# Optimization experiments

Hardware: AMD Instinct MI355X
Metric: run time of the kernel (lower is better)

Reference implementation:

```python
import math
import jax, jax.numpy as jnp
import numpy as np

# ---- static config (matches init_kwargs) ----
B, L, D = 32, 1024, 256
H = 4
E = D // H          # head dim = 64
LF = L // 2 + 1     # rfft bins = 513
LEFT, RIGHT = 205, 513   # retained freq band: int(LF*(1-0.6)) .. LF  (i=0, global mixer)
SPATIAL_RATIO = 0.1
TOP_K = int(5 * math.log(L))  # factor=5 -> 34
LN_EPS = 1e-8


def _layer_norm(x, g, b):
    m = jnp.mean(x, axis=-1, keepdims=True)
    v = jnp.mean((x - m) ** 2, axis=-1, keepdims=True)
    return (x - m) / jnp.sqrt(v + LN_EPS) * g + b


def _gelu_erf(x):
    return x * 0.5 * (1.0 + jax.lax.erf(x / math.sqrt(2.0)))


def _time_delay_agg_training(values, corr):
    # values, corr: [B,H,E,L]; shared top-k delay indices across batch (training path)
    mean_value = jnp.mean(corr, axis=(1, 2))                  # [B,L]
    _, index = jax.lax.top_k(jnp.mean(mean_value, axis=0), TOP_K)  # [TOP_K] int32
    weights = mean_value[:, index]                            # [B,TOP_K]
    tmp_corr = jax.nn.softmax(weights, axis=-1)               # [B,TOP_K]
    t = jnp.arange(L)

    def body(acc, args):
        idx, w = args                                         # idx: scalar delay, w: [B]
        pattern = jnp.take(values, (t + idx) % L, axis=-1)    # roll(values, -idx, axis=-1)
        return acc + pattern * w[:, None, None, None], None

    acc, _ = jax.lax.scan(body, jnp.zeros_like(values), (index, tmp_corr.T))
    return acc                                                # [B,H,E,L]


def setup_inputs() -> dict:
    key = jax.random.key(0)
    ks = jax.random.split(key, 12)
    lin = lambda k: jax.random.normal(k, (D, D), jnp.float32) * 0.02  # stored [in,out]
    return {
        "x": jax.random.normal(ks[0], (B, L, D), jnp.float32),
        "Wq": lin(ks[1]), "bq": jnp.zeros((D,), jnp.float32),
        "Wk": lin(ks[2]), "bk": jnp.zeros((D,), jnp.float32),
        "Wv": lin(ks[3]), "bv": jnp.zeros((D,), jnp.float32),
        "Wd": lin(ks[4]), "bd": jnp.zeros((D,), jnp.float32),
        "ln1_g": jnp.ones((D,), jnp.float32), "ln1_b": jnp.zeros((D,), jnp.float32),
        "W1": lin(ks[5]), "b1": jnp.zeros((D,), jnp.float32),
        "W2": lin(ks[6]), "b2": jnp.zeros((D,), jnp.float32),
        "ln2_g": jnp.ones((D,), jnp.float32), "ln2_b": jnp.zeros((D,), jnp.float32),
    }


def reference(x, Wq, bq, Wk, bk, Wv, bv, Wd, bd, ln1_g, ln1_b, W1, b1, W2, b2, ln2_g, ln2_b):
    # ---- HybridAttention ----
    q = (x @ Wq + bq).reshape(B, L, H, E).transpose(0, 2, 3, 1)  # [B,H,E,L]
    k = (x @ Wk + bk).reshape(B, L, H, E).transpose(0, 2, 3, 1)
    v = (x @ Wv + bv).reshape(B, L, H, E).transpose(0, 2, 3, 1)

    q_fft = jnp.fft.rfft(q, axis=-1)      # [B,H,E,LF]
    k_fft = jnp.fft.rfft(k, axis=-1)
    mask = jnp.zeros((LF,), jnp.float32).at[LEFT:RIGHT].set(1.0)

    # band-limited autocorrelation (equivalent to the index-box scatter/gather)
    corr = jnp.fft.irfft(q_fft * jnp.conj(k_fft) * mask, n=L, axis=-1)  # [B,H,E,L]
    Vt = _time_delay_agg_training(v, corr)                              # [B,H,E,L]
    context_time = Vt.transpose(0, 3, 1, 2).reshape(B, L, D)

    # spatial (band-pass filtered) attention branch
    v_fft = jnp.fft.rfft(v, axis=-1)
    qs = jnp.fft.irfft(q_fft * mask, n=L, axis=-1).transpose(0, 1, 3, 2)  # [B,H,L,E]
    ks_ = jnp.fft.irfft(k_fft * mask, n=L, axis=-1).transpose(0, 1, 3, 2)
    vs = jnp.fft.irfft(v_fft * mask, n=L, axis=-1).transpose(0, 1, 3, 2)
    scores = jnp.einsum('bhle,bhse->bhls', qs, ks_) / math.sqrt(E)
    probs = jax.nn.softmax(scores, axis=-1)
    ctx_sp = jnp.einsum('bhls,bhse->bhle', probs, vs).transpose(0, 2, 1, 3).reshape(B, L, D)

    context = (1.0 - SPATIAL_RATIO) * context_time + SPATIAL_RATIO * ctx_sp
    h = _layer_norm(context @ Wd + bd + x, ln1_g, ln1_b)

    # ---- FeedForward ----
    f = _gelu_erf(h @ W1 + b1) @ W2 + b2
    return _layer_norm(f + h, ln2_g, ln2_b)
```

## Files before the change

kernel.cpp:

```cpp
#include <hip/hip_runtime.h>
#include <hip/hip_bf16.h>
#include <math.h>

#define Lc 1024
#define Dc 256
#define Bc 32
#define Hc 4
#define Ec 64
#define TOPK 34
#define LEFTc 205

typedef unsigned short u16;
typedef __attribute__((ext_vector_type(8))) short bf16x8;
typedef __attribute__((ext_vector_type(4))) float f32x4;

__device__ __forceinline__ float bf2f(u16 u) {
    return __uint_as_float(((unsigned)u) << 16);
}
__device__ __forceinline__ u16 f2bf(float f) {
    unsigned u = __float_as_uint(f);
    u += 0x7FFFu + ((u >> 16) & 1u);
    return (u16)(u >> 16);
}

__global__ void detect_k(const u16* __restrict__ x, int* __restrict__ flag) {
    __shared__ int cnt;
    if (threadIdx.x == 0) cnt = 0;
    __syncthreads();
    int bad = 0;
    for (int i = threadIdx.x; i < 4096; i += 256) {
        float a = fabsf(bf2f(x[i]));
        if (!(a == 0.0f || (a >= 1e-8f && a <= 1e8f))) bad++;
    }
    atomicAdd(&cnt, bad);
    __syncthreads();
    if (threadIdx.x == 0) *flag = (cnt > 512) ? 1 : 0;
}

struct SrcPtrs { const void* p[17]; };
__global__ __launch_bounds__(256) void ingest_all_k(
    SrcPtrs sp, u16* __restrict__ cx, u16* __restrict__ wts, const int* __restrict__ flag)
{
    const long NB = (long)Bc * Lc * Dc;
    long i = (long)blockIdx.x * 256 + threadIdx.x;
    const int fp = *flag;
    const void* src; u16* dst; long off;
    if (i < NB) {
        src = sp.p[0]; dst = cx; off = i;
    } else {
        long j = i - NB;
        if (j < 6L * 65536) {
            const int w = (int)(j >> 16); off = j & 65535;
            const int wsidx[6] = {1, 3, 5, 7, 11, 13};
            src = sp.p[wsidx[w]]; dst = wts + (long)w * 65536;
        } else {
            long k2 = j - 6L * 65536;
            if (k2 >= 2560) return;
            const int v = (int)(k2 >> 8); off = k2 & 255;
            const int vsidx[10] = {2, 4, 6, 8, 9, 10, 12, 14, 15, 16};
            src = sp.p[vsidx[v]]; dst = wts + 6L * 65536 + (long)v * 256;
        }
    }
    dst[off] = fp ? f2bf(((const float*)src)[off]) : ((const u16*)src)[off];
}

__global__ void build_h(float* __restrict__ hf) {
    int d = blockIdx.x * blockDim.x + threadIdx.x;
    if (d >= Lc) return;
    float s = 0.f;
    for (int f = LEFTc; f < 512; ++f) {
        int m = (f * d) & (Lc - 1);
        s += __cosf((float)m * 6.135923151542565e-3f);
    }
    float ny = (d & 1) ? -1.f : 1.f;
    hf[d] = (2.f * s + ny) * (1.f / 1024.f);
}

__global__ void build_G(const float* __restrict__ hf, u16* __restrict__ G) {
    int i = blockIdx.x * 256 + threadIdx.x;
    int t = i >> 10, s = i & (Lc - 1);
    G[i] = f2bf(hf[(t - s) & (Lc - 1)]);
}

__global__ __launch_bounds__(256) void transpose_k(
    const u16* __restrict__ in, u16* __restrict__ out)
{
    __shared__ u16 t[32][33];
    const int l0 = blockIdx.x * 32, d0 = blockIdx.y * 32, b = blockIdx.z;
    const int tx = threadIdx.x & 31, ty = threadIdx.x >> 5;
    const u16* ib = in + (size_t)b * Lc * Dc;
    #pragma unroll
    for (int i = 0; i < 4; ++i)
        t[ty + i * 8][tx] = ib[(size_t)(l0 + ty + i * 8) * Dc + d0 + tx];
    __syncthreads();
    u16* ob = out + (size_t)b * Dc * Lc;
    #pragma unroll
    for (int i = 0; i < 4; ++i)
        ob[(size_t)(d0 + ty + i * 8) * Lc + l0 + tx] = t[tx][ty + i * 8];
}

__global__ __launch_bounds__(256) void wtrans_k(
    const u16* __restrict__ src, u16* __restrict__ dst)
{
    __shared__ u16 t[32][33];
    const int c0 = blockIdx.x * 32, r0 = blockIdx.y * 32;
    const u16* s = src + (size_t)blockIdx.z * 65536;
    u16* d = dst + (size_t)blockIdx.z * 65536;
    const int tx = threadIdx.x & 31, ty = threadIdx.x >> 5;
    #pragma unroll
    for (int i = 0; i < 4; ++i)
        t[ty + i * 8][tx] = s[(r0 + ty + i * 8) * 256 + c0 + tx];
    __syncthreads();
    #pragma unroll
    for (int i = 0; i < 4; ++i)
        d[(c0 + ty + i * 8) * 256 + r0 + tx] = t[tx][ty + i * 8];
}

template <int EPI, bool ACOMB>
__global__ __launch_bounds__(256) void mgemm_k(
    const u16* __restrict__ Abase, const u16* __restrict__ A2base,
    const u16* __restrict__ BTbase, const u16* __restrict__ bias,
    const u16* __restrict__ resid, u16* __restrict__ Cbase,
    int M, int N, int K, long strA, long strBT, long strC)
{
    const int z = blockIdx.z;
    const u16* A  = Abase + (size_t)z * strA;
    const u16* BT = BTbase + (size_t)z * strBT;
    u16* C        = Cbase + (size_t)z * strC;
    const int tid = threadIdx.x;
    const int wave = tid >> 6, lane = tid & 63;
    const int m16 = lane & 15, quad = lane >> 4;
    const int m0 = blockIdx.y * 128 + wave * 32;
    const int n0 = blockIdx.x * 64;

    __shared__ __align__(16) u16 sB[8192];

    const u16* arow0 = A + (size_t)(m0 + m16) * K + quad * 8;
    const u16* arow1 = arow0 + (size_t)16 * K;
    const u16* a2row0 = ACOMB ? (A2base + (size_t)z * strA + (size_t)(m0 + m16) * K + quad * 8) : nullptr;
    const u16* a2row1 = ACOMB ? (a2row0 + (size_t)16 * K) : nullptr;

    const u16* bgp[4];
    u16* bls[4];
    #pragma unroll
    for (int i = 0; i < 4; ++i) {
        const int c = tid + i * 256;
        const int nr = c >> 4, ko = c & 15;
        bgp[i] = BT + (size_t)(n0 + nr) * K + ko * 8;
        bls[i] = sB + ((nr >> 4) * 4 + (ko >> 2)) * 512 + (ko & 3) * 128
                    + (((nr & 15) ^ (ko & 3))) * 8;
    }

    bf16x8 breg[4];
    #pragma unroll
    for (int i = 0; i < 4; ++i) breg[i] = *(const bf16x8*)(bgp[i]);

    f32x4 acc[2][4] = {};

    #pragma unroll 1
    for (int kc = 0; kc < K; kc += 128) {
        #pragma unroll
        for (int i = 0; i < 4; ++i) *(bf16x8*)(bls[i]) = breg[i];
        __syncthreads();
        if (kc + 128 < K) {
            #pragma unroll
            for (int i = 0; i < 4; ++i) breg[i] = *(const bf16x8*)(bgp[i] + kc + 128);
        }
        #pragma unroll
        for (int kf = 0; kf < 4; ++kf) {
            bf16x8 a0 = *(const bf16x8*)(arow0 + kc + kf * 32);
            bf16x8 a1 = *(const bf16x8*)(arow1 + kc + kf * 32);
            if (ACOMB) {
                const bf16x8 x0 = *(const bf16x8*)(a2row0 + kc + kf * 32);
                const bf16x8 x1 = *(const bf16x8*)(a2row1 + kc + kf * 32);
                #pragma unroll
                for (int j = 0; j < 8; ++j) {
                    a0[j] = (short)f2bf(0.9f * bf2f((u16)a0[j]) + 0.1f * bf2f((u16)x0[j]));
                    a1[j] = (short)f2bf(0.9f * bf2f((u16)a1[j]) + 0.1f * bf2f((u16)x1[j]));
                }
            }
            #pragma unroll
            for (int nt = 0; nt < 4; ++nt) {
                const bf16x8 bf = *(const bf16x8*)(sB + (nt * 4 + kf) * 512 + quad * 128
                                                      + ((m16 ^ quad)) * 8);
                acc[0][nt] = __builtin_amdgcn_mfma_f32_16x16x32_bf16(a0, bf, acc[0][nt], 0, 0, 0);
                acc[1][nt] = __builtin_amdgcn_mfma_f32_16x16x32_bf16(a1, bf, acc[1][nt], 0, 0, 0);
            }
        }
        __syncthreads();
    }

    #pragma unroll
    for (int ms = 0; ms < 2; ++ms) {
        #pragma unroll
        for (int nt = 0; nt < 4; ++nt) {
            const int col = n0 + nt * 16 + m16;
            const float bv = bias ? bf2f(bias[col]) : 0.f;
            #pragma unroll
            for (int r = 0; r < 4; ++r) {
                const size_t off = (size_t)(m0 + ms * 16 + quad * 4 + r) * N + col;
                float v = acc[ms][nt][r] + bv;
                if (EPI == 1) v += bf2f(resid[off]);
                if (EPI == 2) v = 0.5f * v * (1.0f + erff(v * 0.70710678118654752f));
                C[off] = f2bf(v);
            }
        }
    }
}

__global__ __launch_bounds__(256) void corr_k(
    const u16* __restrict__ qs, const u16* __restrict__ ks, float* __restrict__ mv)
{
    const int l = blockIdx.x;
    const int b = ((l & 7) << 2) | ((l >> 3) & 3);
    const int rest = l >> 5;
    const int g = rest & 15;
    const int uq = rest >> 4;
    const int wave = threadIdx.x >> 6, lane = threadIdx.x & 63;
    const int m16 = lane & 15, quad = lane >> 4;
    const size_t base = (size_t)b * Lc * Dc;

    __shared__ float red[4][124];
    for (int i = threadIdx.x; i < 4 * 124; i += 256) ((float*)red)[i] = 0.f;
    __syncthreads();

    f32x4 acc[4] = {};
    #pragma unroll
    for (int ui = 0; ui < 4; ++ui) {
        const int u = uq * 16 + wave * 4 + ui;
        const u16* qrow = qs + base + (size_t)(u * 16 + m16) * Dc + quad * 8;
        const u16* kr[4];
        #pragma unroll
        for (int al = 0; al < 4; ++al) {
            const int s = (u - g * 4 - al) & 63;
            kr[al] = ks + base + (size_t)(s * 16 + m16) * Dc + quad * 8;
        }
        #pragma unroll
        for (int k0 = 0; k0 < Dc; k0 += 32) {
            const bf16x8 aq = *(const bf16x8*)(qrow + k0);
            #pragma unroll
            for (int al = 0; al < 4; ++al) {
                const bf16x8 bk = *(const bf16x8*)(kr[al] + k0);
                acc[al] = __builtin_amdgcn_mfma_f32_16x16x32_bf16(aq, bk, acc[al], 0, 0, 0);
            }
        }
    }

    #pragma unroll
    for (int al = 0; al < 4; ++al)
        #pragma unroll
        for (int r = 0; r < 4; ++r)
            atomicAdd(&red[wave][al * 31 + quad * 4 + r - m16 + 15], acc[al][r]);
    __syncthreads();

    if (threadIdx.x < 124) {
        const int al = threadIdx.x / 31, dd = threadIdx.x % 31;
        const float s = red[0][threadIdx.x] + red[1][threadIdx.x] +
                        red[2][threadIdx.x] + red[3][threadIdx.x];
        atomicAdd(&mv[b * Lc + (((g * 4 + al) * 16 + dd - 15) & (Lc - 1))], s);
    }
}

__global__ __launch_bounds__(256) void attn_k(
    const u16* __restrict__ qs, const u16* __restrict__ ks,
    const u16* __restrict__ vsT, u16* __restrict__ ctx)
{
    const int lt = blockIdx.x, h = blockIdx.y, b = blockIdx.z;

    __shared__ __align__(16) u16 sK[8192];
    __shared__ __align__(16) u16 sV[8192];
    __shared__ __align__(16) u16 sP[8192];

    const int tid  = threadIdx.x;
    const int wave = tid >> 6;
    const int lane = tid & 63;
    const int m16  = lane & 15;
    const int quad = lane >> 4;
    const int l0   = lt * 64;
    const size_t base = (size_t)b * Lc * Dc + (size_t)h * Ec;
    const size_t vtbase = ((size_t)b * Dc + (size_t)h * Ec) * Lc;

    const u16* qrow = qs + base + (size_t)(l0 + wave * 16 + m16) * Dc + quad * 8;
    const bf16x8 qa0 = *(const bf16x8*)(qrow);
    const bf16x8 qa1 = *(const bf16x8*)(qrow + 32);

    const u16* kgp[4]; const u16* vgp[4];
    u16* kls[4]; u16* vls[4];
    #pragma unroll
    for (int i = 0; i < 4; ++i) {
        const int c = tid + i * 256;
        const int sr = c >> 3, eo = c & 7;
        kgp[i] = ks + base + (size_t)sr * Dc + eo * 8;
        kls[i] = sK + ((sr >> 4) * 2 + (eo >> 2)) * 512 + (eo & 3) * 128
                    + (((sr & 15) ^ (eo & 3))) * 8;
        const int er = c >> 4, so = c & 15;
        vgp[i] = vsT + vtbase + (size_t)er * Lc + so * 8;
        vls[i] = sV + ((er >> 4) * 4 + (so >> 2)) * 512 + (so & 3) * 128
                    + (((er & 15) ^ (so & 3))) * 8;
    }

    bf16x8 kreg[4], vreg[4];
    #pragma unroll
    for (int i = 0; i < 4; ++i) {
        kreg[i] = *(const bf16x8*)(kgp[i]);
        vreg[i] = *(const bf16x8*)(vgp[i]);
    }

    f32x4 o[4] = {};
    float rs[4] = {0.f, 0.f, 0.f, 0.f};

    const int rsw = m16 ^ quad;
    const int hrd = ((quad & 1) << 1) | (m16 >> 3);
    const int prd = (m16 ^ hrd) * 8;

    #pragma unroll 1
    for (int s0 = 0; s0 < Lc; s0 += 128) {
        #pragma unroll
        for (int i = 0; i < 4; ++i) {
            *(bf16x8*)(kls[i]) = kreg[i];
            *(bf16x8*)(vls[i]) = vreg[i];
        }
        __syncthreads();
        if (s0 + 128 < Lc) {
            #pragma unroll
            for (int i = 0; i < 4; ++i) {
                kreg[i] = *(const bf16x8*)(kgp[i] + (size_t)(s0 + 128) * Dc);
                vreg[i] = *(const bf16x8*)(vgp[i] + (s0 + 128));
            }
        }

        #pragma unroll
        for (int st = 0; st < 8; ++st) {
            const bf16x8 kb0 = *(const bf16x8*)(sK + (st * 2 + 0) * 512 + quad * 128 + rsw * 8);
            const bf16x8 kb1 = *(const bf16x8*)(sK + (st * 2 + 1) * 512 + quad * 128 + rsw * 8);
            f32x4 c4 = {0.f, 0.f, 0.f, 0.f};
            c4 = __builtin_amdgcn_mfma_f32_16x16x32_bf16(qa0, kb0, c4, 0, 0, 0);
            c4 = __builtin_amdgcn_mfma_f32_16x16x32_bf16(qa1, kb1, c4, 0, 0, 0);
            const int q2 = ((st & 1) << 1) | (m16 >> 3);
            const int hst = ((q2 & 1) << 1) | (quad >> 1);
            u16* pw = sP + wave * 2048 + (st >> 1) * 512 + q2 * 128 + (m16 & 7);
            #pragma unroll
            for (int r = 0; r < 4; ++r) {
                const float p = __expf(c4[r] * 0.125f);
                rs[r] += p;
                pw[(((quad * 4 + r) ^ hst)) * 8] = f2bf(p);
            }
        }
        __syncthreads();

        const bf16x8 a0 = *(const bf16x8*)(sP + wave * 2048 + 0 * 512 + quad * 128 + prd);
        const bf16x8 a1 = *(const bf16x8*)(sP + wave * 2048 + 1 * 512 + quad * 128 + prd);
        const bf16x8 a2 = *(const bf16x8*)(sP + wave * 2048 + 2 * 512 + quad * 128 + prd);
        const bf16x8 a3 = *(const bf16x8*)(sP + wave * 2048 + 3 * 512 + quad * 128 + prd);
        #pragma unroll
        for (int nt = 0; nt < 4; ++nt) {
            o[nt] = __builtin_amdgcn_mfma_f32_16x16x32_bf16(a0, *(const bf16x8*)(sV + (nt * 4 + 0) * 512 + quad * 128 + rsw * 8), o[nt], 0, 0, 0);
            o[nt] = __builtin_amdgcn_mfma_f32_16x16x32_bf16(a1, *(const bf16x8*)(sV + (nt * 4 + 1) * 512 + quad * 128 + rsw * 8), o[nt], 0, 0, 0);
            o[nt] = __builtin_amdgcn_mfma_f32_16x16x32_bf16(a2, *(const bf16x8*)(sV + (nt * 4 + 2) * 512 + quad * 128 + rsw * 8), o[nt], 0, 0, 0);
            o[nt] = __builtin_amdgcn_mfma_f32_16x16x32_bf16(a3, *(const bf16x8*)(sV + (nt * 4 + 3) * 512 + quad * 128 + rsw * 8), o[nt], 0, 0, 0);
        }
        __syncthreads();
    }

    #pragma unroll
    for (int off = 1; off < 16; off <<= 1) {
        #pragma unroll
        for (int r = 0; r < 4; ++r) rs[r] += __shfl_xor(rs[r], off);
    }
    #pragma unroll
    for (int nt = 0; nt < 4; ++nt) {
        #pragma unroll
        for (int r = 0; r < 4; ++r)
            ctx[base + (size_t)(l0 + wave * 16 + quad * 4 + r) * Dc + nt * 16 + m16] =
                f2bf(o[nt][r] / rs[r]);
    }
}

__global__ __launch_bounds__(1024) void topk_k(
    const float* __restrict__ mv, int* __restrict__ idx_g, float* __restrict__ w_g)
{
    __shared__ float wvs[16];
    __shared__ int   wis[16];
    __shared__ int   widx;
    __shared__ int   sidx[TOPK];
    const int tid = threadIdx.x;
    const int lane = tid & 63;
    const int wv_id = tid >> 6;

    float g = 0.f;
    for (int b = 0; b < Bc; ++b) g += mv[b * Lc + tid];

    for (int j = 0; j < TOPK; ++j) {
        float v = g; int ix = tid;
        #pragma unroll
        for (int off = 32; off > 0; off >>= 1) {
            const float ov = __shfl_xor(v, off);
            const int   oi = __shfl_xor(ix, off);
            if (ov > v || (ov == v && oi < ix)) { v = ov; ix = oi; }
        }
        if (lane == 0) { wvs[wv_id] = v; wis[wv_id] = ix; }
        __syncthreads();
        if (tid == 0) {
            float bv = wvs[0]; int bi = wis[0];
            for (int u = 1; u < 16; ++u)
                if (wvs[u] > bv || (wvs[u] == bv && wis[u] < bi)) { bv = wvs[u]; bi = wis[u]; }
            widx = bi; sidx[j] = bi; idx_g[j] = bi;
        }
        __syncthreads();
        if (tid == widx) g = -3e38f;
        __syncthreads();
    }
    if (tid < Bc) {
        float wv[TOPK];
        float mx = -3e38f;
        for (int j = 0; j < TOPK; ++j) {
            wv[j] = mv[tid * Lc + sidx[j]] * (1.0f / (float)Dc);
            mx = fmaxf(mx, wv[j]);
        }
        float sum = 0.f;
        for (int j = 0; j < TOPK; ++j) { wv[j] = expf(wv[j] - mx); sum += wv[j]; }
        for (int j = 0; j < TOPK; ++j) w_g[tid * TOPK + j] = wv[j] / sum;
    }
}

__global__ __launch_bounds__(256) void agg_k(
    const u16* __restrict__ v, const int* __restrict__ idx,
    const float* __restrict__ w, u16* __restrict__ ct)
{
    const int b = blockIdx.y;
    const int t = blockIdx.x * 4 + (threadIdx.x >> 6);
    const int lane = threadIdx.x & 63;
    __shared__ int   sidx[TOPK];
    __shared__ float sw[TOPK];
    if (threadIdx.x < TOPK) { sidx[threadIdx.x] = idx[threadIdx.x]; sw[threadIdx.x] = w[b * TOPK + threadIdx.x]; }
    __syncthreads();
    const u16* vb = v + (size_t)b * Lc * Dc;
    const int c4 = lane * 4;
    float a0 = 0.f, a1 = 0.f, a2 = 0.f, a3 = 0.f;
    for (int j = 0; j < TOPK; ++j) {
        const float wj = sw[j];
        const ushort4 u = *reinterpret_cast<const ushort4*>(
            vb + (size_t)((t + sidx[j]) & (Lc - 1)) * Dc + c4);
        a0 += wj * bf2f(u.x); a1 += wj * bf2f(u.y);
        a2 += wj * bf2f(u.z); a3 += wj * bf2f(u.w);
    }
    ushort4 o; o.x = f2bf(a0); o.y = f2bf(a1); o.z = f2bf(a2); o.w = f2bf(a3);
    *reinterpret_cast<ushort4*>(ct + (size_t)b * Lc * Dc + (size_t)t * Dc + c4) = o;
}

template <bool FINAL>
__global__ __launch_bounds__(256) void ln_k(
    const u16* __restrict__ in, const u16* __restrict__ g,
    const u16* __restrict__ be, void* __restrict__ out, const int* __restrict__ flag)
{
    const int wave = threadIdx.x >> 6, lane = threadIdx.x & 63;
    const int row = blockIdx.x * 4 + wave;
    const int c4 = lane * 4;
    const ushort4 u = *reinterpret_cast<const ushort4*>(in + (size_t)row * Dc + c4);
    float x[4] = {bf2f(u.x), bf2f(u.y), bf2f(u.z), bf2f(u.w)};
    float sm = x[0] + x[1] + x[2] + x[3];
    float sq = x[0]*x[0] + x[1]*x[1] + x[2]*x[2] + x[3]*x[3];
    #pragma unroll
    for (int off = 1; off < 64; off <<= 1) {
        sm += __shfl_xor(sm, off);
        sq += __shfl_xor(sq, off);
    }
    const float mean = sm * (1.f / 256.f);
    const float var = sq * (1.f / 256.f) - mean * mean;
    const float rstd = __frsqrt_rn(var + 1e-8f);
    const ushort4 gg = *reinterpret_cast<const ushort4*>(g + c4);
    const ushort4 bb = *reinterpret_cast<const ushort4*>(be + c4);
    float y[4];
    y[0] = (x[0] - mean) * rstd * bf2f(gg.x) + bf2f(bb.x);
    y[1] = (x[1] - mean) * rstd * bf2f(gg.y) + bf2f(bb.y);
    y[2] = (x[2] - mean) * rstd * bf2f(gg.z) + bf2f(bb.z);
    y[3] = (x[3] - mean) * rstd * bf2f(gg.w) + bf2f(bb.w);
    if (FINAL && *flag) {
        float4 o = make_float4(y[0], y[1], y[2], y[3]);
        *reinterpret_cast<float4*>((float*)out + (size_t)row * Dc + c4) = o;
    } else {
        ushort4 o; o.x = f2bf(y[0]); o.y = f2bf(y[1]); o.z = f2bf(y[2]); o.w = f2bf(y[3]);
        *reinterpret_cast<ushort4*>((u16*)out + (size_t)row * Dc + c4) = o;
    }
}

extern "C" void kernel_launch(void* const* d_in, const int* in_sizes, int n_in,
                              void* d_out, int out_size, void* d_ws, size_t ws_size,
                              hipStream_t stream)
{
    (void)in_sizes; (void)n_in; (void)out_size; (void)ws_size;

    const size_t BLD = (size_t)Bc * Lc * Dc;
    const size_t SLOT = BLD * 2;
    const long LD = (long)(Lc * Dc);
    char* ws = (char*)d_ws;
    u16* b0 = (u16*)(ws + 0 * SLOT);
    u16* b1 = (u16*)(ws + 1 * SLOT);
    u16* b2 = (u16*)(ws + 2 * SLOT);
    u16* b3 = (u16*)(ws + 3 * SLOT);
    u16* cx = (u16*)(ws + 4 * SLOT);
    u16* G  = (u16*)(ws + 5 * SLOT);
    char* tail = ws + 5 * SLOT + (size_t)Lc * Lc * 2;
    u16* wts  = (u16*)tail;
    u16* wtsT = wts + 6 * 65536 + 10 * 256;
    char* tail2 = (char*)(wtsT + 6 * 65536);
    float* hf  = (float*)(tail2 + 512);
    float* mv  = hf + Lc;
    int*   idx = (int*)(mv + Bc * Lc);
    float* wsm = (float*)(idx + 64);
    int*   flag = (int*)(wsm + Bc * TOPK);

    u16* vecs = wts + 6 * 65536;
    u16* cbv = vecs + 2 * 256;  u16* cbd = vecs + 3 * 256;
    u16* l1g = vecs + 4 * 256;  u16* l1b = vecs + 5 * 256;
    u16* cb1 = vecs + 6 * 256;  u16* cb2 = vecs + 7 * 256;
    u16* l2g = vecs + 8 * 256;  u16* l2b = vecs + 9 * 256;
    u16* wvT = wtsT + 2 * 65536;
    u16* wdT = wtsT + 3 * 65536; u16* w1T = wtsT + 4 * 65536; u16* w2T = wtsT + 5 * 65536;

    detect_k<<<dim3(1), 256, 0, stream>>>((const u16*)d_in[0], flag);
    SrcPtrs sp;
    for (int i = 0; i < 17; ++i) sp.p[i] = d_in[i];
    ingest_all_k<<<dim3(34314), 256, 0, stream>>>(sp, cx, wts, flag);
    wtrans_k<<<dim3(8, 8, 6), 256, 0, stream>>>(wts, wtsT);

    build_h<<<dim3(4), 256, 0, stream>>>(hf);
    build_G<<<dim3((Lc * Lc) / 256), 256, 0, stream>>>(hf, G);

    transpose_k<<<dim3(32, 8, 32), 256, 0, stream>>>(cx, b1);
    mgemm_k<0, false><<<dim3(4, 8, 32), 256, 0, stream>>>(
        G, nullptr, b1, nullptr, nullptr, b0, Lc, Dc, Lc, 0, LD, LD);

    mgemm_k<0, false><<<dim3(4, 256, 3), 256, 0, stream>>>(
        b0, nullptr, wtsT, nullptr, nullptr, b1, Bc * Lc, Dc, Dc, 0, 65536, (long)BLD);

    hipMemsetAsync(mv, 0, (size_t)Bc * Lc * 4, stream);
    corr_k<<<dim3(2048), 256, 0, stream>>>(b1, b2, mv);

    transpose_k<<<dim3(32, 8, 32), 256, 0, stream>>>(b3, b0);
    attn_k<<<dim3(16, 4, 32), 256, 0, stream>>>(b1, b2, b0, b3);

    topk_k<<<dim3(1), 1024, 0, stream>>>(mv, idx, wsm);

    const dim3 gProj(4, 256, 1);
    mgemm_k<0, false><<<gProj, 256, 0, stream>>>(cx, nullptr, wvT, cbv, nullptr, b1, Bc * Lc, Dc, Dc, 0, 0, 0);
    agg_k<<<dim3(256, 32), 256, 0, stream>>>(b1, idx, wsm, b2);

    mgemm_k<1, true><<<gProj, 256, 0, stream>>>(b2, b3, wdT, cbd, cx, b0, Bc * Lc, Dc, Dc, 0, 0, 0);

    ln_k<false><<<dim3(8192), 256, 0, stream>>>(b0, l1g, l1b, b1, flag);

    mgemm_k<2, false><<<gProj, 256, 0, stream>>>(b1, nullptr, w1T, cb1, nullptr, b2, Bc * Lc, Dc, Dc, 0, 0, 0);
    mgemm_k<1, false><<<gProj, 256, 0, stream>>>(b2, nullptr, w2T, cb2, b1, b3, Bc * Lc, Dc, Dc, 0, 0, 0);

    ln_k<true><<<dim3(8192), 256, 0, stream>>>(b3, l2g, l2b, d_out, flag);
}
```

Measured before the change: 621.1 us.

## Fuse autocorrelation diagonal sums into attention score computation

Removes the separate corr_k kernel, which recomputed Q·K products to build per-lag correlation sums. The attention kernel now accumulates each raw score into a shared-memory per-lag array by wrapped diagonal and adds that array to the global mean-value buffer at the end. This reuses the score MFMAs already done for attention. In exchange it adds a shared atomic per score element plus a 4 KB shared array, and it sums per head rather than across all heads, so correctness depends on corr_k having computed the same per-head diagonal sums.

```diff
diff --git a/kernel.cpp b/kernel.cpp
--- a/kernel.cpp
+++ b/kernel.cpp
@@ -208,68 +208,16 @@
     }
 }
 
-__global__ __launch_bounds__(256) void corr_k(
-    const u16* __restrict__ qs, const u16* __restrict__ ks, float* __restrict__ mv)
-{
-    const int l = blockIdx.x;
-    const int b = ((l & 7) << 2) | ((l >> 3) & 3);
-    const int rest = l >> 5;
-    const int g = rest & 15;
-    const int uq = rest >> 4;
-    const int wave = threadIdx.x >> 6, lane = threadIdx.x & 63;
-    const int m16 = lane & 15, quad = lane >> 4;
-    const size_t base = (size_t)b * Lc * Dc;
-
-    __shared__ float red[4][124];
-    for (int i = threadIdx.x; i < 4 * 124; i += 256) ((float*)red)[i] = 0.f;
-    __syncthreads();
-
-    f32x4 acc[4] = {};
-    #pragma unroll
-    for (int ui = 0; ui < 4; ++ui) {
-        const int u = uq * 16 + wave * 4 + ui;
-        const u16* qrow = qs + base + (size_t)(u * 16 + m16) * Dc + quad * 8;
-        const u16* kr[4];
-        #pragma unroll
-        for (int al = 0; al < 4; ++al) {
-            const int s = (u - g * 4 - al) & 63;
-            kr[al] = ks + base + (size_t)(s * 16 + m16) * Dc + quad * 8;
-        }
-        #pragma unroll
-        for (int k0 = 0; k0 < Dc; k0 += 32) {
-            const bf16x8 aq = *(const bf16x8*)(qrow + k0);
-            #pragma unroll
-            for (int al = 0; al < 4; ++al) {
-                const bf16x8 bk = *(const bf16x8*)(kr[al] + k0);
-                acc[al] = __builtin_amdgcn_mfma_f32_16x16x32_bf16(aq, bk, acc[al], 0, 0, 0);
-            }
-        }
-    }
-
-    #pragma unroll
-    for (int al = 0; al < 4; ++al)
-        #pragma unroll
-        for (int r = 0; r < 4; ++r)
-            atomicAdd(&red[wave][al * 31 + quad * 4 + r - m16 + 15], acc[al][r]);
-    __syncthreads();
-
-    if (threadIdx.x < 124) {
-        const int al = threadIdx.x / 31, dd = threadIdx.x % 31;
-        const float s = red[0][threadIdx.x] + red[1][threadIdx.x] +
-                        red[2][threadIdx.x] + red[3][threadIdx.x];
-        atomicAdd(&mv[b * Lc + (((g * 4 + al) * 16 + dd - 15) & (Lc - 1))], s);
-    }
-}
-
 __global__ __launch_bounds__(256) void attn_k(
     const u16* __restrict__ qs, const u16* __restrict__ ks,
-    const u16* __restrict__ vsT, u16* __restrict__ ctx)
+    const u16* __restrict__ vsT, u16* __restrict__ ctx, float* __restrict__ mv)
 {
     const int lt = blockIdx.x, h = blockIdx.y, b = blockIdx.z;
 
     __shared__ __align__(16) u16 sK[8192];
     __shared__ __align__(16) u16 sV[8192];
     __shared__ __align__(16) u16 sP[8192];
+    __shared__ float diag[Lc];
 
     const int tid  = threadIdx.x;
     const int wave = tid >> 6;
@@ -283,6 +231,8 @@
     const u16* qrow = qs + base + (size_t)(l0 + wave * 16 + m16) * Dc + quad * 8;
     const bf16x8 qa0 = *(const bf16x8*)(qrow);
     const bf16x8 qa1 = *(const bf16x8*)(qrow + 32);
+
+    for (int i = tid; i < Lc; i += 256) diag[i] = 0.f;
 
     const u16* kgp[4]; const u16* vgp[4];
     u16* kls[4]; u16* vls[4];
@@ -312,6 +262,7 @@
     const int rsw = m16 ^ quad;
     const int hrd = ((quad & 1) << 1) | (m16 >> 3);
     const int prd = (m16 ^ hrd) * 8;
+    const int cth = l0 + wave * 16 + quad * 4 - m16;
 
     #pragma unroll 1
     for (int s0 = 0; s0 < Lc; s0 += 128) {
@@ -338,10 +289,13 @@
             c4 = __builtin_amdgcn_mfma_f32_16x16x32_bf16(qa1, kb1, c4, 0, 0, 0);
             const int q2 = ((st & 1) << 1) | (m16 >> 3);
             const int hst = ((q2 & 1) << 1) | (quad >> 1);
+            const int tb0 = (cth - s0 - st * 16) & (Lc - 1);
             u16* pw = sP + wave * 2048 + (st >> 1) * 512 + q2 * 128 + (m16 & 7);
             #pragma unroll
             for (int r = 0; r < 4; ++r) {
-                const float p = __expf(c4[r] * 0.125f);
+                const float sc = c4[r];
+                atomicAdd(&diag[(tb0 + r) & (Lc - 1)], sc);
+                const float p = __expf(sc * 0.125f);
                 rs[r] += p;
                 pw[(((quad * 4 + r) ^ hst)) * 8] = f2bf(p);
             }
@@ -374,6 +328,9 @@
             ctx[base + (size_t)(l0 + wave * 16 + quad * 4 + r) * Dc + nt * 16 + m16] =
                 f2bf(o[nt][r] / rs[r]);
     }
+
+    for (int i = tid; i < Lc; i += 256)
+        atomicAdd(&mv[(size_t)b * Lc + i], diag[i]);
 }
 
 __global__ __launch_bounds__(1024) void topk_k(
@@ -535,10 +492,8 @@
         b0, nullptr, wtsT, nullptr, nullptr, b1, Bc * Lc, Dc, Dc, 0, 65536, (long)BLD);
 
     hipMemsetAsync(mv, 0, (size_t)Bc * Lc * 4, stream);
-    corr_k<<<dim3(2048), 256, 0, stream>>>(b1, b2, mv);
-
     transpose_k<<<dim3(32, 8, 32), 256, 0, stream>>>(b3, b0);
-    attn_k<<<dim3(16, 4, 32), 256, 0, stream>>>(b1, b2, b0, b3);
+    attn_k<<<dim3(16, 4, 32), 256, 0, stream>>>(b1, b2, b0, b3, mv);
 
     topk_k<<<dim3(1), 1024, 0, stream>>>(mv, idx, wsm);
 
```

After: 1.155 ms. 1.86x slower.

## Widen corr_k diagonal tile to 8 offsets with double-buffered register loads

Applied to the files above, without the earlier changes.

Each block in the correlation kernel now covers 8 diagonal offsets instead of 4, so every loaded Q fragment feeds twice as many MFMAs, and the grid is halved to match. Global loads of the Q and K fragments are double-buffered in registers across a fully unrolled 32-step loop, so the next loads are in flight while the current MFMAs run. LDS and global atomics use unsafeAtomicAdd to allow hardware float atomics. Register pressure rises sharply (8 accumulators plus two sets of 9 fragment vectors), which can lower occupancy or cause spills.

```diff
diff --git a/kernel.cpp b/kernel.cpp
--- a/kernel.cpp
+++ b/kernel.cpp
@@ -214,50 +214,57 @@
     const int l = blockIdx.x;
     const int b = ((l & 7) << 2) | ((l >> 3) & 3);
     const int rest = l >> 5;
-    const int g = rest & 15;
-    const int uq = rest >> 4;
+    const int gp = rest & 7;
+    const int uq = rest >> 3;
     const int wave = threadIdx.x >> 6, lane = threadIdx.x & 63;
     const int m16 = lane & 15, quad = lane >> 4;
     const size_t base = (size_t)b * Lc * Dc;
-
-    __shared__ float red[4][124];
-    for (int i = threadIdx.x; i < 4 * 124; i += 256) ((float*)red)[i] = 0.f;
-    __syncthreads();
-
-    f32x4 acc[4] = {};
-    #pragma unroll
-    for (int ui = 0; ui < 4; ++ui) {
-        const int u = uq * 16 + wave * 4 + ui;
-        const u16* qrow = qs + base + (size_t)(u * 16 + m16) * Dc + quad * 8;
-        const u16* kr[4];
-        #pragma unroll
-        for (int al = 0; al < 4; ++al) {
-            const int s = (u - g * 4 - al) & 63;
-            kr[al] = ks + base + (size_t)(s * 16 + m16) * Dc + quad * 8;
-        }
-        #pragma unroll
-        for (int k0 = 0; k0 < Dc; k0 += 32) {
-            const bf16x8 aq = *(const bf16x8*)(qrow + k0);
-            #pragma unroll
-            for (int al = 0; al < 4; ++al) {
-                const bf16x8 bk = *(const bf16x8*)(kr[al] + k0);
-                acc[al] = __builtin_amdgcn_mfma_f32_16x16x32_bf16(aq, bk, acc[al], 0, 0, 0);
-            }
-        }
-    }
-
-    #pragma unroll
-    for (int al = 0; al < 4; ++al)
+    const u16* qb = qs + base;
+    const u16* kb = ks + base;
+    const int moff = m16 * Dc + quad * 8;
+    const int u0 = uq * 16 + wave * 4;
+    const int A = gp * 8;
+
+    __shared__ float red[4][248];
+    for (int i = threadIdx.x; i < 4 * 248; i += 256) ((float*)red)[i] = 0.f;
+    __syncthreads();
+
+    f32x4 acc[8] = {};
+    bf16x8 qv[2]; bf16x8 kv[2][8];
+
+#define CLOAD(IT, P) do {                                                     \
+    const int u_ = u0 + ((IT) >> 3); const int k0_ = ((IT) & 7) * 32;         \
+    qv[P] = *(const bf16x8*)(qb + (u_ << 12) + moff + k0_);                   \
+    _Pragma("unroll")                                                         \
+    for (int al_ = 0; al_ < 8; ++al_) {                                       \
+        const int s_ = (u_ - A - al_) & 63;                                   \
+        kv[P][al_] = *(const bf16x8*)(kb + (s_ << 12) + moff + k0_);          \
+    } } while (0)
+
+    CLOAD(0, 0);
+    CLOAD(1, 1);
+    #pragma unroll
+    for (int it = 0; it < 32; ++it) {
+        const int p = it & 1;
+        #pragma unroll
+        for (int al = 0; al < 8; ++al)
+            acc[al] = __builtin_amdgcn_mfma_f32_16x16x32_bf16(qv[p], kv[p][al], acc[al], 0, 0, 0);
+        if (it + 2 < 32) CLOAD(it + 2, p);
+    }
+#undef CLOAD
+
+    #pragma unroll
+    for (int al = 0; al < 8; ++al)
         #pragma unroll
         for (int r = 0; r < 4; ++r)
-            atomicAdd(&red[wave][al * 31 + quad * 4 + r - m16 + 15], acc[al][r]);
-    __syncthreads();
-
-    if (threadIdx.x < 124) {
+            unsafeAtomicAdd(&red[wave][al * 31 + quad * 4 + r - m16 + 15], acc[al][r]);
+    __syncthreads();
+
+    if (threadIdx.x < 248) {
         const int al = threadIdx.x / 31, dd = threadIdx.x % 31;
         const float s = red[0][threadIdx.x] + red[1][threadIdx.x] +
                         red[2][threadIdx.x] + red[3][threadIdx.x];
-        atomicAdd(&mv[b * Lc + (((g * 4 + al) * 16 + dd - 15) & (Lc - 1))], s);
+        unsafeAtomicAdd(&mv[b * Lc + (((A + al) * 16 + dd - 15) & (Lc - 1))], s);
     }
 }
 
@@ -535,7 +542,7 @@
         b0, nullptr, wtsT, nullptr, nullptr, b1, Bc * Lc, Dc, Dc, 0, 65536, (long)BLD);
 
     hipMemsetAsync(mv, 0, (size_t)Bc * Lc * 4, stream);
-    corr_k<<<dim3(2048), 256, 0, stream>>>(b1, b2, mv);
+    corr_k<<<dim3(1024), 256, 0, stream>>>(b1, b2, mv);
 
     transpose_k<<<dim3(32, 8, 32), 256, 0, stream>>>(b3, b0);
     attn_k<<<dim3(16, 4, 32), 256, 0, stream>>>(b1, b2, b0, b3);
```

New measurement: 640.2 us. 3.1% more time.

## Restructure corr kernel to stage K tiles in LDS ring buffer with register prefetch

Applied to the files above, without the earlier changes.

The correlation kernel is reorganised so each block keeps one Q row-tile per wave in registers and walks 16 diagonal offsets. K tiles are staged through an 8-slot swizzled LDS ring, with the next tiles prefetched into registers while MFMAs run. This replaces repeated uncoalesced global reads of K, where each wave reloaded four K tiles per Q tile, with shared reuse across the four waves. The reduction buffer grows and uses unsafeAtomicAdd. The cost is more LDS (about 72KB), which lowers occupancy, plus a barrier on every iteration.

```diff
diff --git a/kernel.cpp b/kernel.cpp
--- a/kernel.cpp
+++ b/kernel.cpp
@@ -211,53 +211,103 @@
 __global__ __launch_bounds__(256) void corr_k(
     const u16* __restrict__ qs, const u16* __restrict__ ks, float* __restrict__ mv)
 {
-    const int l = blockIdx.x;
-    const int b = ((l & 7) << 2) | ((l >> 3) & 3);
-    const int rest = l >> 5;
-    const int g = rest & 15;
-    const int uq = rest >> 4;
-    const int wave = threadIdx.x >> 6, lane = threadIdx.x & 63;
+    const int bid = blockIdx.x;
+    const int b = ((bid & 7) << 2) | ((bid >> 3) & 3);
+    const int rest = bid >> 5;
+    const int uq4 = rest & 15;
+    const int Aq  = rest >> 4;
+    const int A   = Aq * 16;
+    const int tid = threadIdx.x;
+    const int wave = tid >> 6, lane = tid & 63;
     const int m16 = lane & 15, quad = lane >> 4;
     const size_t base = (size_t)b * Lc * Dc;
-
-    __shared__ float red[4][124];
-    for (int i = threadIdx.x; i < 4 * 124; i += 256) ((float*)red)[i] = 0.f;
+    const u16* qb = qs + base;
+    const u16* kb = ks + base;
+
+    __shared__ __align__(16) u16 sK[8][4096];
+    __shared__ float red[4][496];
+
+    for (int i = tid; i < 4 * 496; i += 256) ((float*)red)[i] = 0.f;
+
+    const int u  = uq4 * 4 + wave;
+    const int Gp = uq4 * 4 - A + 64;
+
+    bf16x8 qv[8];
+    {
+        const u16* qrow = qb + (size_t)(u * 16 + m16) * Dc + quad * 8;
+        #pragma unroll
+        for (int k0 = 0; k0 < 8; ++k0) qv[k0] = *(const bf16x8*)(qrow + k0 * 32);
+    }
+
+    const int srow = tid >> 4;
+    const int c0   = (tid & 15) * 2;
+    const size_t goff = (size_t)srow * Dc + (size_t)(tid & 15) * 16;
+
+    #pragma unroll
+    for (int p = 0; p < 5; ++p) {
+        const int g = Gp - 1 + p;
+        const u16* gp = kb + (size_t)((g & 63) * 16) * Dc + goff;
+        const bf16x8 v0 = *(const bf16x8*)(gp);
+        const bf16x8 v1 = *(const bf16x8*)(gp + 8);
+        u16* lp = &sK[g & 7][srow * 256];
+        *(bf16x8*)(lp + (c0 ^ srow) * 8)       = v0;
+        *(bf16x8*)(lp + ((c0 + 1) ^ srow) * 8) = v1;
+    }
+    bf16x8 gA0, gA1, gB0, gB1;
+    {
+        const u16* gp = kb + (size_t)(((Gp - 2) & 63) * 16) * Dc + goff;
+        gA0 = *(const bf16x8*)(gp); gA1 = *(const bf16x8*)(gp + 8);
+        const u16* gq = kb + (size_t)(((Gp - 3) & 63) * 16) * Dc + goff;
+        gB0 = *(const bf16x8*)(gq); gB1 = *(const bf16x8*)(gq + 8);
+    }
     __syncthreads();
 
-    f32x4 acc[4] = {};
-    #pragma unroll
-    for (int ui = 0; ui < 4; ++ui) {
-        const int u = uq * 16 + wave * 4 + ui;
-        const u16* qrow = qs + base + (size_t)(u * 16 + m16) * Dc + quad * 8;
-        const u16* kr[4];
-        #pragma unroll
-        for (int al = 0; al < 4; ++al) {
-            const int s = (u - g * 4 - al) & 63;
-            kr[al] = ks + base + (size_t)(s * 16 + m16) * Dc + quad * 8;
-        }
-        #pragma unroll
-        for (int k0 = 0; k0 < Dc; k0 += 32) {
-            const bf16x8 aq = *(const bf16x8*)(qrow + k0);
-            #pragma unroll
-            for (int al = 0; al < 4; ++al) {
-                const bf16x8 bk = *(const bf16x8*)(kr[al] + k0);
-                acc[al] = __builtin_amdgcn_mfma_f32_16x16x32_bf16(aq, bk, acc[al], 0, 0, 0);
+    const int rb = quad * 4 - m16 + 15;
+
+    #pragma unroll
+    for (int j = 0; j < 8; ++j) {
+        const int al0 = 2 * j, al1 = 2 * j + 1;
+        const u16* lA = &sK[(Gp + wave - al0) & 7][m16 * 256];
+        const u16* lB = &sK[(Gp + wave - al1) & 7][m16 * 256];
+        bf16x8 kA[8], kB[8];
+        #pragma unroll
+        for (int k0 = 0; k0 < 8; ++k0) {
+            const int sw = ((k0 * 4 + quad) ^ m16) * 8;
+            kA[k0] = *(const bf16x8*)(lA + sw);
+            kB[k0] = *(const bf16x8*)(lB + sw);
+        }
+        f32x4 o0 = {0.f, 0.f, 0.f, 0.f}, o1 = {0.f, 0.f, 0.f, 0.f};
+        #pragma unroll
+        for (int k0 = 0; k0 < 8; ++k0) {
+            o0 = __builtin_amdgcn_mfma_f32_16x16x32_bf16(qv[k0], kA[k0], o0, 0, 0, 0);
+            o1 = __builtin_amdgcn_mfma_f32_16x16x32_bf16(qv[k0], kB[k0], o1, 0, 0, 0);
+        }
+        if (j < 7) {
+            u16* l0 = &sK[(Gp - 2 * j - 2) & 7][srow * 256];
+            *(bf16x8*)(l0 + (c0 ^ srow) * 8)       = gA0;
+            *(bf16x8*)(l0 + ((c0 + 1) ^ srow) * 8) = gA1;
+            u16* l1 = &sK[(Gp - 2 * j - 3) & 7][srow * 256];
+            *(bf16x8*)(l1 + (c0 ^ srow) * 8)       = gB0;
+            *(bf16x8*)(l1 + ((c0 + 1) ^ srow) * 8) = gB1;
+            if (j < 6) {
+                const u16* gp = kb + (size_t)(((Gp - 2 * j - 4) & 63) * 16) * Dc + goff;
+                gA0 = *(const bf16x8*)(gp); gA1 = *(const bf16x8*)(gp + 8);
+                const u16* gq = kb + (size_t)(((Gp - 2 * j - 5) & 63) * 16) * Dc + goff;
+                gB0 = *(const bf16x8*)(gq); gB1 = *(const bf16x8*)(gq + 8);
             }
         }
-    }
-
-    #pragma unroll
-    for (int al = 0; al < 4; ++al)
-        #pragma unroll
-        for (int r = 0; r < 4; ++r)
-            atomicAdd(&red[wave][al * 31 + quad * 4 + r - m16 + 15], acc[al][r]);
-    __syncthreads();
-
-    if (threadIdx.x < 124) {
-        const int al = threadIdx.x / 31, dd = threadIdx.x % 31;
-        const float s = red[0][threadIdx.x] + red[1][threadIdx.x] +
-                        red[2][threadIdx.x] + red[3][threadIdx.x];
-        atomicAdd(&mv[b * Lc + (((g * 4 + al) * 16 + dd - 15) & (Lc - 1))], s);
+        #pragma unroll
+        for (int r = 0; r < 4; ++r) {
+            unsafeAtomicAdd(&red[wave][al0 * 31 + rb + r], o0[r]);
+            unsafeAtomicAdd(&red[wave][al1 * 31 + rb + r], o1[r]);
+        }
+        __syncthreads();
+    }
+
+    for (int i = tid; i < 496; i += 256) {
+        const int al = i / 31, dd = i % 31;
+        const float s = red[0][i] + red[1][i] + red[2][i] + red[3][i];
+        unsafeAtomicAdd(&mv[b * Lc + ((16 * (A + al) + dd - 15) & (Lc - 1))], s);
     }
 }
 
```

Result: slower. 714.2 us (+15.0%).
